# Kernel optimization log

Hardware: AMD Instinct MI355X
Metric: run time of the kernel (lower is better)

## Reference

```python
import jax, jax.numpy as jnp
import numpy as np

B, S, HID = 2, 2048, 2048
NH, HD = 16, 128
EPS = 1e-5


def setup_inputs() -> dict:
    key = jax.random.key(0)
    ks = jax.random.split(key, 6)
    std = 1.0 / np.sqrt(HID)
    x = jax.random.normal(ks[0], (B, S, HID), dtype=jnp.float32)
    Wq = jax.random.normal(ks[1], (HID, NH * HD), dtype=jnp.float32) * std
    Wk = jax.random.normal(ks[2], (HID, NH * HD), dtype=jnp.float32) * std
    Wv = jax.random.normal(ks[3], (HID, NH * HD), dtype=jnp.float32) * std
    Wo = jax.random.normal(ks[4], (NH * HD, HID), dtype=jnp.float32) * std
    rms_w = jnp.ones((HID,), dtype=jnp.float32)
    # RoPE tables: freqs_cis.real / .imag, shape [S, HD//2]
    inv_freq = 1.0 / (10000.0 ** (np.arange(0, HD, 2, dtype=np.float32) / HD))
    angles = jnp.asarray(np.arange(S, dtype=np.float32)[:, None] * inv_freq[None, :])
    cos = jnp.cos(angles)
    sin = jnp.sin(angles)
    return {"x": x, "rms_w": rms_w, "Wq": Wq, "Wk": Wk, "Wv": Wv, "Wo": Wo,
            "cos": cos, "sin": sin}


def _rmsnorm(x, w):
    var = jnp.mean(jnp.square(x), axis=-1, keepdims=True)
    return x * jax.lax.rsqrt(var + EPS) * w


def _rope(t, cos, sin):
    # t: [B, S, H, D]; cos/sin: [S, D/2]  (rotate-half RoPE)
    d2 = t.shape[-1] // 2
    t1, t2 = t[..., :d2], t[..., d2:]
    c = cos[None, :, None, :]
    s = sin[None, :, None, :]
    return jnp.concatenate([t1 * c - t2 * s, t2 * c + t1 * s], axis=-1)


def reference(x, rms_w, Wq, Wk, Wv, Wo, cos, sin):
    residual = x
    h = _rmsnorm(x, rms_w)
    q = (h @ Wq).reshape(B, S, NH, HD)
    k = (h @ Wk).reshape(B, S, NH, HD)
    v = (h @ Wv).reshape(B, S, NH, HD)
    q = _rope(q, cos, sin)
    k = _rope(k, cos, sin)
    # [B, H, S, D]
    q = q.transpose(0, 2, 1, 3)
    k = k.transpose(0, 2, 1, 3)
    v = v.transpose(0, 2, 1, 3)
    scale = 1.0 / jnp.sqrt(jnp.float32(HD))
    scores = jnp.einsum('bhqd,bhkd->bhqk', q, k) * scale
    causal = jnp.tril(jnp.ones((S, S), dtype=bool))
    scores = jnp.where(causal[None, None], scores, jnp.finfo(scores.dtype).min)
    probs = jax.nn.softmax(scores, axis=-1)
    attn = jnp.einsum('bhqk,bhkd->bhqd', probs, v)
    attn = attn.transpose(0, 2, 1, 3).reshape(B, S, NH * HD)
    out = attn @ Wo
    return (residual + out).astype(x.dtype)
```

## Files before the change

kernel.cpp:

```cpp
#include <hip/hip_runtime.h>

#define HID   2048
#define S_LEN 2048
#define NHEAD 16
#define HD    128
#define NKV   2048

typedef __attribute__((ext_vector_type(8))) short   short8;
typedef __attribute__((ext_vector_type(4))) float   floatx4;

__device__ __forceinline__ unsigned short f2bf(float f) {
    union { float f; unsigned u; } v; v.f = f;
    unsigned r = v.u + 0x7fffu + ((v.u >> 16) & 1u);
    return (unsigned short)(r >> 16);
}
__device__ __forceinline__ float bf2f(unsigned short h) {
    union { unsigned u; float f; } v; v.u = ((unsigned)h) << 16; return v.f;
}

__device__ __forceinline__ void async16(void* lds, const void* g) {
    __builtin_amdgcn_global_load_lds(
        (const __attribute__((address_space(1))) unsigned int*)g,
        (__attribute__((address_space(3))) unsigned int*)lds, 16, 0, 0);
}

__global__ __launch_bounds__(256) void rmsnorm_kernel(const float* __restrict__ x,
        const float* __restrict__ w, unsigned short* __restrict__ h) {
    const int row = blockIdx.x;
    const int t = threadIdx.x;
    const float* xr = x + (size_t)row * HID;
    float4 v0 = *(const float4*)(xr + t * 4);
    float4 v1 = *(const float4*)(xr + 1024 + t * 4);
    float ss = v0.x*v0.x + v0.y*v0.y + v0.z*v0.z + v0.w*v0.w
             + v1.x*v1.x + v1.y*v1.y + v1.z*v1.z + v1.w*v1.w;
    #pragma unroll
    for (int off = 1; off < 64; off <<= 1) ss += __shfl_xor(ss, off, 64);
    __shared__ float red[4];
    if ((t & 63) == 0) red[t >> 6] = ss;
    __syncthreads();
    float tot = red[0] + red[1] + red[2] + red[3];
    float inv = rsqrtf(tot * (1.0f / HID) + 1e-5f);
    float4 w0 = *(const float4*)(w + t * 4);
    float4 w1 = *(const float4*)(w + 1024 + t * 4);
    ushort4 o0, o1;
    o0.x = f2bf(v0.x * inv * w0.x); o0.y = f2bf(v0.y * inv * w0.y);
    o0.z = f2bf(v0.z * inv * w0.z); o0.w = f2bf(v0.w * inv * w0.w);
    o1.x = f2bf(v1.x * inv * w1.x); o1.y = f2bf(v1.y * inv * w1.y);
    o1.z = f2bf(v1.z * inv * w1.z); o1.w = f2bf(v1.w * inv * w1.w);
    *(ushort4*)(h + (size_t)row * HID + t * 4) = o0;
    *(ushort4*)(h + (size_t)row * HID + 1024 + t * 4) = o1;
}

__global__ __launch_bounds__(256) void wtrans_kernel(const float* __restrict__ Wq,
        const float* __restrict__ Wk, const float* __restrict__ Wv,
        const float* __restrict__ Wo,
        unsigned short* __restrict__ wt_qkv, unsigned short* __restrict__ wt_o) {
    __shared__ float tile[64][65];
    const int sel = blockIdx.z;
    const float* W = (sel == 0) ? Wq : (sel == 1) ? Wk : (sel == 2) ? Wv : Wo;
    const int n0 = blockIdx.x * 64, k0 = blockIdx.y * 64;
    const int t = threadIdx.x;
    const int col = t & 63, r4 = t >> 6;
    #pragma unroll
    for (int i = 0; i < 16; ++i) {
        int rr = r4 + i * 4;
        tile[rr][col] = W[(size_t)(k0 + rr) * NKV + n0 + col];
    }
    __syncthreads();
    #pragma unroll
    for (int i = 0; i < 16; ++i) {
        int rr = r4 + i * 4;
        unsigned short v = f2bf(tile[col][rr]);
        if (sel < 3) wt_qkv[((size_t)(sel * 2048 + n0 + rr)) * HID + k0 + col] = v;
        else         wt_o  [((size_t)(n0 + rr)) * HID + k0 + col] = v;
    }
}

__device__ __forceinline__ void gemm_body(const unsigned short* __restrict__ A,
        const unsigned short* __restrict__ Bt, int K, int rowBase, int colBase,
        unsigned short* As, unsigned short* Bs, floatx4 acc[4][4]) {
    const int t = threadIdx.x;
    const int lane = t & 63, w = t >> 6;
    const int wm = (w >> 1) * 64, wsel = w & 1;
    const int lr = lane & 15, quad = lane >> 4;
    #pragma unroll
    for (int mi = 0; mi < 4; ++mi)
        #pragma unroll
        for (int ni = 0; ni < 4; ++ni) {
            acc[mi][ni][0] = 0.f; acc[mi][ni][1] = 0.f;
            acc[mi][ni][2] = 0.f; acc[mi][ni][3] = 0.f;
        }
    for (int k0 = 0; k0 < K; k0 += 64) {
        __syncthreads();
        #pragma unroll
        for (int c = 0; c < 4; ++c) {
            int e = (c * 256 + t) * 8;
            int r = e >> 6;
            int chunk = ((e >> 3) & 7) ^ (r & 7);
            async16(As + e, A  + (size_t)(rowBase + r) * K + k0 + chunk * 8);
            async16(Bs + e, Bt + (size_t)(colBase + r) * K + k0 + chunk * 8);
        }
        __syncthreads();
        #pragma unroll
        for (int ks = 0; ks < 2; ++ks) {
            short8 af[4], bfr[4];
            int cp = (ks * 4 + quad) ^ (lr & 7);
            #pragma unroll
            for (int i = 0; i < 4; ++i)
                af[i] = *(const short8*)(As + (wm + i * 16 + lr) * 64 + cp * 8);
            #pragma unroll
            for (int i = 0; i < 4; ++i)
                bfr[i] = *(const short8*)(Bs + (i * 32 + wsel * 16 + lr) * 64 + cp * 8);
            #pragma unroll
            for (int mi = 0; mi < 4; ++mi)
                #pragma unroll
                for (int ni = 0; ni < 4; ++ni)
                    acc[mi][ni] = __builtin_amdgcn_mfma_f32_16x16x32_bf16(
                        af[mi], bfr[ni], acc[mi][ni], 0, 0, 0);
        }
    }
}

__global__ __launch_bounds__(256) void gemm_qkv_kernel(const unsigned short* __restrict__ h,
        const unsigned short* __restrict__ wt, const float* __restrict__ cosp,
        const float* __restrict__ sinp, unsigned short* __restrict__ qk,
        unsigned short* __restrict__ vT) {
    __shared__ __align__(16) unsigned short As[128 * 64];
    __shared__ __align__(16) unsigned short Bs[128 * 64];
    floatx4 acc[4][4];
    const int rowBase = blockIdx.y * 128, colBase = blockIdx.x * 128;
    gemm_body(h, wt, HID, rowBase, colBase, As, Bs, acc);
    const int t = threadIdx.x, lane = t & 63, w = t >> 6;
    const int wm = (w >> 1) * 64, wsel = w & 1;
    const int lr = lane & 15, quad = lane >> 4;
    const int sel = colBase >> 11;
    const int hh = (colBase >> 7) & 15;
    #pragma unroll
    for (int mi = 0; mi < 4; ++mi) {
        int row0 = rowBase + wm + mi * 16 + quad * 4;
        int b = row0 >> 11, s0 = row0 & 2047;
        if (sel < 2) {
            unsigned short* base = qk + (size_t)sel * 8388608
                                 + ((size_t)(b * NHEAD + hh) * S_LEN) * HD;
            #pragma unroll
            for (int ni = 0; ni < 2; ++ni) {
                int d = ni * 32 + wsel * 16 + lr;
                #pragma unroll
                for (int r = 0; r < 4; ++r) {
                    int s = s0 + r;
                    float c  = cosp[s * 64 + d];
                    float sn = sinp[s * 64 + d];
                    float v1 = acc[mi][ni][r], v2 = acc[mi][ni + 2][r];
                    base[(size_t)s * HD + d]      = f2bf(v1 * c - v2 * sn);
                    base[(size_t)s * HD + d + 64] = f2bf(v2 * c + v1 * sn);
                }
            }
        } else {
            #pragma unroll
            for (int ni = 0; ni < 4; ++ni) {
                int d = ni * 32 + wsel * 16 + lr;
                ushort4 pk;
                pk.x = f2bf(acc[mi][ni][0]); pk.y = f2bf(acc[mi][ni][1]);
                pk.z = f2bf(acc[mi][ni][2]); pk.w = f2bf(acc[mi][ni][3]);
                *(ushort4*)(vT + ((size_t)(b * NHEAD + hh) * HD + d) * S_LEN + s0) = pk;
            }
        }
    }
}

__global__ __launch_bounds__(256, 2) void attn_kernel(const unsigned short* __restrict__ q,
        const unsigned short* __restrict__ k, const unsigned short* __restrict__ vT,
        unsigned short* __restrict__ out) {
    __shared__ __align__(16) unsigned short Kd[2][64 * 128];
    __shared__ __align__(16) unsigned short Vd[2][128 * 64];
    __shared__ __align__(16) unsigned short Ps[4][32 * 64];

    const int id = blockIdx.x;
    const int half = id >> 8;
    const int r8 = id & 255;
    const int bh = r8 >> 3;
    const int j  = r8 & 7;
    const int qi2 = half ? j : (15 - j);

    const unsigned short* qb = q  + (size_t)bh * S_LEN * HD;
    const unsigned short* kb = k  + (size_t)bh * S_LEN * HD;
    const unsigned short* vb = vT + (size_t)bh * HD * S_LEN;
    const int t = threadIdx.x, lane = t & 63, w = t >> 6;
    const int lr = lane & 15, quad = lane >> 4;
    const float SC = 0.1275174855f;

    short8 qf[2][4];
    #pragma unroll
    for (int mi = 0; mi < 2; ++mi) {
        int qrow = qi2 * 128 + mi * 64 + w * 16 + lr;
        #pragma unroll
        for (int ks = 0; ks < 4; ++ks) {
            short8 raw = *(const short8*)(qb + (size_t)qrow * HD + ks * 32 + quad * 8);
            #pragma unroll
            for (int jj = 0; jj < 8; ++jj)
                qf[mi][ks][jj] = (short)f2bf(bf2f((unsigned short)raw[jj]) * SC);
        }
    }
    floatx4 o[2][8];
    #pragma unroll
    for (int mi = 0; mi < 2; ++mi)
        #pragma unroll
        for (int i = 0; i < 8; ++i) { o[mi][i][0]=0.f; o[mi][i][1]=0.f; o[mi][i][2]=0.f; o[mi][i][3]=0.f; }
    float rs[2][4] = {{0.f,0.f,0.f,0.f},{0.f,0.f,0.f,0.f}};

    const int ktmax = 2 * qi2 + 1;

    auto stage = [&](int kt2, int buf) {
        unsigned short* Kb = &Kd[buf][0];
        unsigned short* Vb = &Vd[buf][0];
        #pragma unroll
        for (int c = 0; c < 4; ++c) {
            int e = (c * 256 + t) * 8;
            int kr = e >> 7;
            int kch = ((e >> 3) & 15) ^ (kr & 15);
            async16(Kb + e, kb + (size_t)(kt2 * 64 + kr) * HD + kch * 8);
            int vr = e >> 6;
            int vch = ((e >> 3) & 7) ^ (vr & 7);
            async16(Vb + e, vb + (size_t)vr * S_LEN + kt2 * 64 + vch * 8);
        }
    };

    auto tilework = [&](int kt, bool maskf) {
        const unsigned short* Ksb = &Kd[kt & 1][0];
        const unsigned short* Vsb = &Vd[kt & 1][0];
        floatx4 sc[2][4];
        #pragma unroll
        for (int mi = 0; mi < 2; ++mi)
            #pragma unroll
            for (int ni = 0; ni < 4; ++ni) { sc[mi][ni][0]=0.f; sc[mi][ni][1]=0.f; sc[mi][ni][2]=0.f; sc[mi][ni][3]=0.f; }
        #pragma unroll
        for (int ks = 0; ks < 4; ++ks) {
            #pragma unroll
            for (int ni = 0; ni < 4; ++ni) {
                int row = ni * 16 + lr;
                int cp = (ks * 4 + quad) ^ (lr & 15);
                short8 kf = *(const short8*)(Ksb + row * 128 + cp * 8);
                sc[0][ni] = __builtin_amdgcn_mfma_f32_16x16x32_bf16(qf[0][ks], kf, sc[0][ni], 0, 0, 0);
                sc[1][ni] = __builtin_amdgcn_mfma_f32_16x16x32_bf16(qf[1][ks], kf, sc[1][ni], 0, 0, 0);
            }
        }
        #pragma unroll
        for (int mi = 0; mi < 2; ++mi) {
            int row_out = qi2 * 128 + mi * 64 + w * 16 + quad * 4;
            #pragma unroll
            for (int ni = 0; ni < 4; ++ni) {
                int key = kt * 64 + ni * 16 + lr;
                #pragma unroll
                for (int r = 0; r < 4; ++r) {
                    float p = exp2f(sc[mi][ni][r]);
                    if (maskf && key > row_out + r) p = 0.f;
                    rs[mi][r] += p;
                    int prow = mi * 16 + quad * 4 + r;
                    int chunk = (ni * 2 + (lr >> 3)) ^ (prow & 7);
                    Ps[w][prow * 64 + chunk * 8 + (lr & 7)] =
                        (unsigned short)(__float_as_uint(p) >> 16);
                }
            }
        }
        #pragma unroll
        for (int ks2 = 0; ks2 < 2; ++ks2) {
            int pcp = (ks2 * 4 + quad) ^ (lr & 7);
            short8 pa0 = *(const short8*)(&Ps[w][(lr) * 64 + pcp * 8]);
            short8 pa1 = *(const short8*)(&Ps[w][(16 + lr) * 64 + pcp * 8]);
            #pragma unroll
            for (int nt = 0; nt < 8; ++nt) {
                int row = nt * 16 + lr;
                int vcp = (ks2 * 4 + quad) ^ (lr & 7);
                short8 vf = *(const short8*)(Vsb + row * 64 + vcp * 8);
                o[0][nt] = __builtin_amdgcn_mfma_f32_16x16x32_bf16(pa0, vf, o[0][nt], 0, 0, 0);
                o[1][nt] = __builtin_amdgcn_mfma_f32_16x16x32_bf16(pa1, vf, o[1][nt], 0, 0, 0);
            }
        }
    };

    stage(0, 0);
    int kt = 0;
    for (; kt < 2 * qi2; ++kt) {
        __syncthreads();
        stage(kt + 1, (kt + 1) & 1);
        tilework(kt, false);
    }
    for (; kt <= ktmax; ++kt) {
        __syncthreads();
        if (kt < ktmax) stage(kt + 1, (kt + 1) & 1);
        tilework(kt, true);
    }

    float rl[2][4];
    #pragma unroll
    for (int mi = 0; mi < 2; ++mi)
        #pragma unroll
        for (int r = 0; r < 4; ++r) {
            float s2 = rs[mi][r];
            #pragma unroll
            for (int off = 1; off < 16; off <<= 1) s2 += __shfl_xor(s2, off, 64);
            rl[mi][r] = 1.0f / s2;
        }
    const int b = bh >> 4, hh = bh & 15;
    #pragma unroll
    for (int mi = 0; mi < 2; ++mi) {
        size_t orow0 = (size_t)b * S_LEN + qi2 * 128 + mi * 64 + w * 16 + quad * 4;
        #pragma unroll
        for (int nt = 0; nt < 8; ++nt) {
            int col = hh * HD + nt * 16 + lr;
            #pragma unroll
            for (int r = 0; r < 4; ++r)
                out[(orow0 + r) * NKV + col] = f2bf(o[mi][nt][r] * rl[mi][r]);
        }
    }
}

__global__ __launch_bounds__(256) void gemm_out_kernel(const unsigned short* __restrict__ attn,
        const unsigned short* __restrict__ wto, const float* __restrict__ x,
        float* __restrict__ out) {
    __shared__ __align__(16) unsigned short As[128 * 64];
    __shared__ __align__(16) unsigned short Bs[128 * 64];
    floatx4 acc[4][4];
    const int rowBase = blockIdx.y * 128, colBase = blockIdx.x * 128;
    gemm_body(attn, wto, NKV, rowBase, colBase, As, Bs, acc);
    const int t = threadIdx.x, lane = t & 63, w = t >> 6;
    const int wm = (w >> 1) * 64, wsel = w & 1;
    const int lr = lane & 15, quad = lane >> 4;
    #pragma unroll
    for (int mi = 0; mi < 4; ++mi) {
        int row0 = rowBase + wm + mi * 16 + quad * 4;
        #pragma unroll
        for (int ni = 0; ni < 4; ++ni) {
            int col = colBase + ni * 32 + wsel * 16 + lr;
            #pragma unroll
            for (int r = 0; r < 4; ++r) {
                size_t off = (size_t)(row0 + r) * HID + col;
                out[off] = acc[mi][ni][r] + x[off];
            }
        }
    }
}

extern "C" void kernel_launch(void* const* d_in, const int* in_sizes, int n_in,
                              void* d_out, int out_size, void* d_ws, size_t ws_size,
                              hipStream_t stream) {
    const float* x     = (const float*)d_in[0];
    const float* rms_w = (const float*)d_in[1];
    const float* Wq    = (const float*)d_in[2];
    const float* Wk    = (const float*)d_in[3];
    const float* Wv    = (const float*)d_in[4];
    const float* Wo    = (const float*)d_in[5];
    const float* cosp  = (const float*)d_in[6];
    const float* sinp  = (const float*)d_in[7];
    float* out = (float*)d_out;

    unsigned short* ws   = (unsigned short*)d_ws;
    unsigned short* h    = ws;
    unsigned short* wtq  = ws + 8388608;
    unsigned short* wto  = ws + 20971520;
    unsigned short* qk   = ws + 25165824;
    unsigned short* vT   = ws + 41943040;
    unsigned short* attn = ws + 50331648;

    rmsnorm_kernel<<<4096, 256, 0, stream>>>(x, rms_w, h);
    wtrans_kernel<<<dim3(32, 32, 4), 256, 0, stream>>>(Wq, Wk, Wv, Wo, wtq, wto);
    gemm_qkv_kernel<<<dim3(48, 32), 256, 0, stream>>>(h, wtq, cosp, sinp, qk, vT);
    attn_kernel<<<512, 256, 0, stream>>>(qk, qk + 8388608, vT, attn);
    gemm_out_kernel<<<dim3(16, 32), 256, 0, stream>>>(attn, wto, x, out);
}
```

Measured before the change: 411.2 us.

## Balance causal attention work by splitting paired query tiles across two blocks

Each attention block now processes a heavy and a light causal query tile together. The key range of the pair is split between two role blocks, so every block handles the same number of 64-key tiles. Because the softmax has no running max, each block writes unnormalized bf16 partial outputs and row sums. A new combine kernel adds the two partials and normalizes them. The aim is to remove the tail imbalance from causal masking, at the cost of an extra kernel launch, extra partial-buffer traffic, and bf16 rounding of the partials.

```diff
diff --git a/kernel.cpp b/kernel.cpp
--- a/kernel.cpp
+++ b/kernel.cpp
@@ -170,17 +170,22 @@
 
 __global__ __launch_bounds__(256, 2) void attn_kernel(const unsigned short* __restrict__ q,
         const unsigned short* __restrict__ k, const unsigned short* __restrict__ vT,
-        unsigned short* __restrict__ out) {
+        unsigned short* __restrict__ Opart, float* __restrict__ lpart) {
     __shared__ __align__(16) unsigned short Kd[2][64 * 128];
     __shared__ __align__(16) unsigned short Vd[2][128 * 64];
     __shared__ __align__(16) unsigned short Ps[4][32 * 64];
 
     const int id = blockIdx.x;
-    const int half = id >> 8;
-    const int r8 = id & 255;
-    const int bh = r8 >> 3;
-    const int j  = r8 & 7;
-    const int qi2 = half ? j : (15 - j);
+    const int bh   = id >> 4;
+    const int j    = (id >> 1) & 7;
+    const int role = id & 1;
+
+    const int qtA = 15 - j, qtB = j;
+    const int n1 = 16 - j;
+    const int n2 = j + 1;
+    const int segqt[2] = {qtA, qtB};
+    const int segk0[2] = {role ? n1 : 0, role ? n2 : 0};
+    const int seglen[2] = {n1, n2};
 
     const unsigned short* qb = q  + (size_t)bh * S_LEN * HD;
     const unsigned short* kb = k  + (size_t)bh * S_LEN * HD;
@@ -190,25 +195,28 @@
     const float SC = 0.1275174855f;
 
     short8 qf[2][4];
+    floatx4 o[2][8];
+    float rs[2][4];
     #pragma unroll
     for (int mi = 0; mi < 2; ++mi) {
-        int qrow = qi2 * 128 + mi * 64 + w * 16 + lr;
-        #pragma unroll
-        for (int ks = 0; ks < 4; ++ks) {
-            short8 raw = *(const short8*)(qb + (size_t)qrow * HD + ks * 32 + quad * 8);
-            #pragma unroll
-            for (int jj = 0; jj < 8; ++jj)
-                qf[mi][ks][jj] = (short)f2bf(bf2f((unsigned short)raw[jj]) * SC);
-        }
-    }
-    floatx4 o[2][8];
-    #pragma unroll
-    for (int mi = 0; mi < 2; ++mi)
         #pragma unroll
         for (int i = 0; i < 8; ++i) { o[mi][i][0]=0.f; o[mi][i][1]=0.f; o[mi][i][2]=0.f; o[mi][i][3]=0.f; }
-    float rs[2][4] = {{0.f,0.f,0.f,0.f},{0.f,0.f,0.f,0.f}};
-
-    const int ktmax = 2 * qi2 + 1;
+        rs[mi][0]=0.f; rs[mi][1]=0.f; rs[mi][2]=0.f; rs[mi][3]=0.f;
+    }
+
+    auto loadq = [&](int qt) {
+        #pragma unroll
+        for (int mi = 0; mi < 2; ++mi) {
+            int qrow = qt * 128 + mi * 64 + w * 16 + lr;
+            #pragma unroll
+            for (int ks = 0; ks < 4; ++ks) {
+                short8 raw = *(const short8*)(qb + (size_t)qrow * HD + ks * 32 + quad * 8);
+                #pragma unroll
+                for (int jj = 0; jj < 8; ++jj)
+                    qf[mi][ks][jj] = (short)f2bf(bf2f((unsigned short)raw[jj]) * SC);
+            }
+        }
+    };
 
     auto stage = [&](int kt2, int buf) {
         unsigned short* Kb = &Kd[buf][0];
@@ -225,9 +233,9 @@
         }
     };
 
-    auto tilework = [&](int kt, bool maskf) {
-        const unsigned short* Ksb = &Kd[kt & 1][0];
-        const unsigned short* Vsb = &Vd[kt & 1][0];
+    auto tilework = [&](int qt, int kt, int buf, bool maskf) {
+        const unsigned short* Ksb = &Kd[buf][0];
+        const unsigned short* Vsb = &Vd[buf][0];
         floatx4 sc[2][4];
         #pragma unroll
         for (int mi = 0; mi < 2; ++mi)
@@ -246,7 +254,7 @@
         }
         #pragma unroll
         for (int mi = 0; mi < 2; ++mi) {
-            int row_out = qi2 * 128 + mi * 64 + w * 16 + quad * 4;
+            int row_out = qt * 128 + mi * 64 + w * 16 + quad * 4;
             #pragma unroll
             for (int ni = 0; ni < 4; ++ni) {
                 int key = kt * 64 + ni * 16 + lr;
@@ -278,40 +286,70 @@
         }
     };
 
-    stage(0, 0);
-    int kt = 0;
-    for (; kt < 2 * qi2; ++kt) {
-        __syncthreads();
-        stage(kt + 1, (kt + 1) & 1);
-        tilework(kt, false);
-    }
-    for (; kt <= ktmax; ++kt) {
-        __syncthreads();
-        if (kt < ktmax) stage(kt + 1, (kt + 1) & 1);
-        tilework(kt, true);
-    }
-
-    float rl[2][4];
-    #pragma unroll
-    for (int mi = 0; mi < 2; ++mi)
-        #pragma unroll
-        for (int r = 0; r < 4; ++r) {
-            float s2 = rs[mi][r];
-            #pragma unroll
-            for (int off = 1; off < 16; off <<= 1) s2 += __shfl_xor(s2, off, 64);
-            rl[mi][r] = 1.0f / s2;
-        }
+    auto flushseg = [&](int qt) {
+        unsigned short* ob = Opart + (size_t)role * 8388608
+                           + ((size_t)(bh * 16 + qt) * 128) * 128;
+        float* lb = lpart + role * 65536 + (bh * 16 + qt) * 128;
+        #pragma unroll
+        for (int mi = 0; mi < 2; ++mi) {
+            int qrow0 = mi * 64 + w * 16 + quad * 4;
+            #pragma unroll
+            for (int r = 0; r < 4; ++r) {
+                float s2 = rs[mi][r];
+                #pragma unroll
+                for (int off = 1; off < 16; off <<= 1) s2 += __shfl_xor(s2, off, 64);
+                if (lr == 0) lb[qrow0 + r] = s2;
+            }
+            #pragma unroll
+            for (int nt = 0; nt < 8; ++nt) {
+                int col = nt * 16 + lr;
+                #pragma unroll
+                for (int r = 0; r < 4; ++r)
+                    ob[(size_t)(qrow0 + r) * 128 + col] = f2bf(o[mi][nt][r]);
+            }
+            #pragma unroll
+            for (int i = 0; i < 8; ++i) { o[mi][i][0]=0.f; o[mi][i][1]=0.f; o[mi][i][2]=0.f; o[mi][i][3]=0.f; }
+            rs[mi][0]=0.f; rs[mi][1]=0.f; rs[mi][2]=0.f; rs[mi][3]=0.f;
+        }
+    };
+
+    stage(segk0[0], 0);
+    int g = 0;
+    for (int s = 0; s < 2; ++s) {
+        loadq(segqt[s]);
+        const int qt = segqt[s], k0 = segk0[s], len = seglen[s];
+        for (int i = 0; i < len; ++i, ++g) {
+            __syncthreads();
+            int ns = s, nidx = i + 1;
+            if (nidx == len) { ns = s + 1; nidx = 0; }
+            if (ns < 2) stage(segk0[ns] + nidx, (g + 1) & 1);
+            int kt = k0 + i;
+            tilework(qt, kt, g & 1, kt >= 2 * qt);
+        }
+        flushseg(qt);
+    }
+}
+
+__global__ __launch_bounds__(256) void combine_kernel(const unsigned short* __restrict__ Opart,
+        const float* __restrict__ lpart, unsigned short* __restrict__ attn) {
+    const int T = blockIdx.x;
+    const int bh = T >> 4, qt = T & 15;
     const int b = bh >> 4, hh = bh & 15;
-    #pragma unroll
-    for (int mi = 0; mi < 2; ++mi) {
-        size_t orow0 = (size_t)b * S_LEN + qi2 * 128 + mi * 64 + w * 16 + quad * 4;
-        #pragma unroll
-        for (int nt = 0; nt < 8; ++nt) {
-            int col = hh * HD + nt * 16 + lr;
-            #pragma unroll
-            for (int r = 0; r < 4; ++r)
-                out[(orow0 + r) * NKV + col] = f2bf(o[mi][nt][r] * rl[mi][r]);
-        }
+    const int t = threadIdx.x;
+    const int qrow = t >> 1, half = t & 1;
+    float rl = 1.0f / (lpart[T * 128 + qrow] + lpart[65536 + T * 128 + qrow]);
+    const unsigned short* pa = Opart + ((size_t)T * 128 + qrow) * 128 + half * 64;
+    const unsigned short* pb = Opart + 8388608 + ((size_t)T * 128 + qrow) * 128 + half * 64;
+    unsigned short* po = attn + ((size_t)(b * S_LEN + qt * 128 + qrow)) * NKV + hh * HD + half * 64;
+    #pragma unroll
+    for (int c = 0; c < 8; ++c) {
+        short8 a8 = *(const short8*)(pa + c * 8);
+        short8 b8 = *(const short8*)(pb + c * 8);
+        short8 o8;
+        #pragma unroll
+        for (int jj = 0; jj < 8; ++jj)
+            o8[jj] = (short)f2bf((bf2f((unsigned short)a8[jj]) + bf2f((unsigned short)b8[jj])) * rl);
+        *(short8*)(po + c * 8) = o8;
     }
 }
 
@@ -361,10 +399,13 @@
     unsigned short* qk   = ws + 25165824;
     unsigned short* vT   = ws + 41943040;
     unsigned short* attn = ws + 50331648;
+    unsigned short* Opart = ws;
+    float* lpart = (float*)(ws + 16777216);
 
     rmsnorm_kernel<<<4096, 256, 0, stream>>>(x, rms_w, h);
     wtrans_kernel<<<dim3(32, 32, 4), 256, 0, stream>>>(Wq, Wk, Wv, Wo, wtq, wto);
     gemm_qkv_kernel<<<dim3(48, 32), 256, 0, stream>>>(h, wtq, cosp, sinp, qk, vT);
-    attn_kernel<<<512, 256, 0, stream>>>(qk, qk + 8388608, vT, attn);
+    attn_kernel<<<512, 256, 0, stream>>>(qk, qk + 8388608, vT, Opart, lpart);
+    combine_kernel<<<512, 256, 0, stream>>>(Opart, lpart, attn);
     gemm_out_kernel<<<dim3(16, 32), 256, 0, stream>>>(attn, wto, x, out);
 }
```

After: 417.9 us. No clear change (+1.6%).
